# Optimization experiments

Hardware: AMD Instinct MI355X
Metric: run time of the kernel (lower is better)

Reference implementation:

```python
import jax, jax.numpy as jnp
import numpy as np

N, E = 50000, 800000
IN, HID, OUT, HEADS = 256, 128, 256, 4
CAT = HEADS * HID  # 512


def _gat(x, ei_src, ei_dst, W, a_src, a_dst, b, heads, out_ch, concat):
    """PyG-style GATConv with self-loops. x:[N,F]; returns [N,heads*out_ch] or [N,out_ch]."""
    n = x.shape[0]
    loop = jnp.arange(n, dtype=ei_src.dtype)
    src = jnp.concatenate([ei_src, loop])
    dst = jnp.concatenate([ei_dst, loop])
    h = (x @ W).reshape(n, heads, out_ch)              # [N,H,C]
    al_s = jnp.einsum('nhc,hc->nh', h, a_src)          # [N,H]
    al_d = jnp.einsum('nhc,hc->nh', h, a_dst)
    e = jax.nn.leaky_relu(al_s[src] + al_d[dst], 0.2)  # [E',H]
    emax = jax.ops.segment_max(e, dst, num_segments=n)
    ee = jnp.exp(e - emax[dst])
    denom = jax.ops.segment_sum(ee, dst, num_segments=n)
    alpha = ee / (denom[dst] + 1e-16)                  # segment softmax over incoming edges
    out = jax.ops.segment_sum(h[src] * alpha[:, :, None], dst, num_segments=n)  # [N,H,C]
    out = out.reshape(n, heads * out_ch) if concat else out.mean(axis=1)
    return out + b


def setup_inputs() -> dict:
    key = jax.random.key(0)
    ks = jax.random.split(key, 20)
    g = lambda k, shape, fan: (jax.random.normal(k, shape, jnp.float32) / np.sqrt(fan)).astype(jnp.float32)
    return {
        'x': jax.random.normal(ks[0], (N, IN), jnp.float32),
        'edge_index': jax.random.randint(ks[1], (2, E), 0, N, dtype=jnp.int32),
        # GAT layer 1: IN -> HID x 4 heads, concat
        'W1': g(ks[2], (IN, CAT), IN), 'a_src1': g(ks[3], (HEADS, HID), HID),
        'a_dst1': g(ks[4], (HEADS, HID), HID), 'b1': jnp.zeros((CAT,), jnp.float32),
        # GAT layer 2: CAT -> HID x 4 heads, concat
        'W2': g(ks[5], (CAT, CAT), CAT), 'a_src2': g(ks[6], (HEADS, HID), HID),
        'a_dst2': g(ks[7], (HEADS, HID), HID), 'b2': jnp.zeros((CAT,), jnp.float32),
        # GAT layer 3: CAT -> OUT, 1 head, no concat
        'W3': g(ks[8], (CAT, OUT), CAT), 'a_src3': g(ks[9], (1, OUT), OUT),
        'a_dst3': g(ks[10], (1, OUT), OUT), 'b3': jnp.zeros((OUT,), jnp.float32),
        # response_generator MLP: OUT -> 2*HID -> HID -> OUT
        'M1': g(ks[11], (OUT, 2 * HID), OUT), 'mb1': jnp.zeros((2 * HID,), jnp.float32),
        'M2': g(ks[12], (2 * HID, HID), 2 * HID), 'mb2': jnp.zeros((HID,), jnp.float32),
        'M3': g(ks[13], (HID, OUT), HID), 'mb3': jnp.zeros((OUT,), jnp.float32),
    }


def reference(x, edge_index, W1, a_src1, a_dst1, b1, W2, a_src2, a_dst2, b2,
              W3, a_src3, a_dst3, b3, M1, mb1, M2, mb2, M3, mb3):
    src, dst = edge_index[0], edge_index[1]
    h = _gat(x, src, dst, W1, a_src1, a_dst1, b1, HEADS, HID, True)
    h = jax.nn.elu(h)  # dropout is identity in eval mode
    h = _gat(h, src, dst, W2, a_src2, a_dst2, b2, HEADS, HID, True)
    h = jax.nn.elu(h)
    h = _gat(h, src, dst, W3, a_src3, a_dst3, b3, 1, OUT, False)
    # response generator MLP (dropout identity in eval)
    r = jax.nn.relu(h @ M1 + mb1)
    r = jax.nn.relu(r @ M2 + mb2)
    return r @ M3 + mb3
```

## Files before the change

kernel.cpp:

```cpp
#include <hip/hip_runtime.h>
#include <cstdint>
#include <cstddef>

#define HEADS  4
#define HIDC   128
#define CATF   512
#define IN_F   256
#define OUT_F  256

typedef _Float16 f16x8 __attribute__((ext_vector_type(8)));
typedef _Float16 f16x4 __attribute__((ext_vector_type(4)));
typedef float f32x4  __attribute__((ext_vector_type(4)));

__device__ __forceinline__ void async16(const void* g, void* l) {
    __builtin_amdgcn_global_load_lds((const __attribute__((address_space(1))) void*)g,
                                     (__attribute__((address_space(3))) void*)l, 16, 0, 0);
}

__global__ void init_counts(int* cnt, int N) {
    int i = blockIdx.x * blockDim.x + threadIdx.x;
    if (i < N) cnt[i] = 1;
}

__global__ void count_dst(const int* __restrict__ dst, int E, int* cnt) {
    int i = blockIdx.x * blockDim.x + threadIdx.x;
    if (i < E) atomicAdd(&cnt[dst[i]], 1);
}

__global__ void scan_partial(const int* __restrict__ cnt, int* excl, int* bsum, int N) {
    __shared__ int tmp[256];
    int i = blockIdx.x * 256 + threadIdx.x;
    int v = (i < N) ? cnt[i] : 0;
    tmp[threadIdx.x] = v;
    __syncthreads();
    for (int off = 1; off < 256; off <<= 1) {
        int t = ((int)threadIdx.x >= off) ? tmp[threadIdx.x - off] : 0;
        __syncthreads();
        tmp[threadIdx.x] += t;
        __syncthreads();
    }
    if (i < N) excl[i] = tmp[threadIdx.x] - v;
    if (threadIdx.x == 255) bsum[blockIdx.x] = tmp[255];
}

__global__ void scan_bsums(int* bsum, int nb) {
    __shared__ int tmp[256];
    int v = ((int)threadIdx.x < nb) ? bsum[threadIdx.x] : 0;
    tmp[threadIdx.x] = v;
    __syncthreads();
    for (int off = 1; off < 256; off <<= 1) {
        int t = ((int)threadIdx.x >= off) ? tmp[threadIdx.x - off] : 0;
        __syncthreads();
        tmp[threadIdx.x] += t;
        __syncthreads();
    }
    if ((int)threadIdx.x < nb) bsum[threadIdx.x] = tmp[threadIdx.x] - v;
}

__global__ void add_carry(int* indptr, int* pos, const int* __restrict__ bsum, int N, int total) {
    int i = blockIdx.x * blockDim.x + threadIdx.x;
    if (i < N) {
        int v = indptr[i] + bsum[i >> 8];
        indptr[i] = v;
        pos[i] = v;
    }
    if (i == 0) indptr[N] = total;
}

__global__ void scatter_edges(const int* __restrict__ src, const int* __restrict__ dst,
                              int E, int N, int* pos, int* esrc) {
    int i = blockIdx.x * blockDim.x + threadIdx.x;
    int total = E + N;
    if (i >= total) return;
    int s, d;
    if (i < E) { s = src[i]; d = dst[i]; }
    else       { s = i - E;  d = s; }
    int p = atomicAdd(&pos[d], 1);
    esrc[p] = s;
}

__global__ void conv_h16(const float* __restrict__ in, _Float16* __restrict__ out, long n4) {
    long i = (long)blockIdx.x * blockDim.x + threadIdx.x;
    if (i >= n4) return;
    float4 v = ((const float4*)in)[i];
    f16x4 o = { (_Float16)v.x, (_Float16)v.y, (_Float16)v.z, (_Float16)v.w };
    ((f16x4*)out)[i] = o;
}

struct WDesc { const float* W; _Float16* hi; _Float16* lo; int K; int N; int off; };
struct WPack { WDesc d[6]; int total; };
__global__ void conv_w_all(WPack p) {
    int idx = blockIdx.x * blockDim.x + threadIdx.x;
    if (idx >= p.total) return;
    int wi = 0;
    while (wi < 5 && idx >= p.d[wi + 1].off) wi++;
    const WDesc& w = p.d[wi];
    int li = idx - w.off;
    int n = li / w.K, k = li - n * w.K;
    float v = w.W[(size_t)k * w.N + n];
    _Float16 h = (_Float16)v;
    w.hi[(size_t)n * w.K + k] = h;
    if (w.lo) w.lo[(size_t)n * w.K + k] = (_Float16)(v - (float)h);
}

__global__ void zero2(float* a, float* b, int n) {
    int i = blockIdx.x * blockDim.x + threadIdx.x;
    if (i < n) { a[i] = 0.f; b[i] = 0.f; }
}

#define TM 128
#define TN 128
#define TK 32
template <int MODE, int NMF, int ATTN>
__global__ __launch_bounds__(256) void gemm_bt(
        const _Float16* __restrict__ A,
        const _Float16* __restrict__ Bh, const _Float16* __restrict__ Bl,
        const float* __restrict__ bias,
        float* __restrict__ out_f, _Float16* __restrict__ out_h16,
        const float* __restrict__ asrc, const float* __restrict__ adst,
        float* __restrict__ al_s, float* __restrict__ al_d,
        int M, int N, int K, int act) {
    __shared__ __align__(16) _Float16 sA[2][TM * TK], sBh[2][TN * TK];
    __shared__ __align__(16) _Float16 sBl[NMF == 2 ? 2 * TN * TK : 16];
    __shared__ float sred[ATTN ? TM * 4 : 4];
    int tid = threadIdx.x;
    int wave = tid >> 6, lane = tid & 63;
    int m0 = blockIdx.y * TM, n0 = blockIdx.x * TN;
    int wm = wave >> 1, wn = wave & 1;
    int srow = lane >> 2;
    int skel = (lane & 3) * 8;
    int fr = lane & 15, quad = lane >> 4;

    f32x4 acc[4][4];
#pragma unroll
    for (int i = 0; i < 4; i++)
#pragma unroll
        for (int j = 0; j < 4; j++) acc[i][j] = (f32x4){0.f, 0.f, 0.f, 0.f};

    auto stage = [&](int buf, int k0) {
#pragma unroll
        for (int c = 0; c < 2; c++) {
            int chunk = wave * 2 + c;
            int r = chunk * 16 + srow;
            int gmA = m0 + r; if (gmA >= M) gmA = M - 1;
            int gnB = n0 + r;
            size_t aoff = (size_t)gmA * K + k0 + skel;
            size_t boff = (size_t)gnB * K + k0 + skel;
            int ldso = chunk * 512;
            async16(A + aoff, &sA[buf][ldso]);
            async16(Bh + boff, &sBh[buf][ldso]);
            if (NMF == 2) async16(Bl + boff, &sBl[buf * (TN * TK) + ldso]);
        }
    };

    const int nsteps = K / TK;
    stage(0, 0);
    int cur = 0;
    for (int s = 0; s < nsteps; ++s, cur ^= 1) {
        if (s + 1 < nsteps) {
            stage(cur ^ 1, (s + 1) * TK);
            if (NMF == 2) asm volatile("s_waitcnt vmcnt(6)" ::: "memory");
            else          asm volatile("s_waitcnt vmcnt(4)" ::: "memory");
        } else {
            asm volatile("s_waitcnt vmcnt(0)" ::: "memory");
        }
        __builtin_amdgcn_s_barrier();
        __builtin_amdgcn_sched_barrier(0);

        f16x8 fa[4], fbh[4], fbl[4];
#pragma unroll
        for (int i = 0; i < 4; i++) {
            int ra = (wm * 64 + i * 16 + fr) * TK + quad * 8;
            int rb = (wn * 64 + i * 16 + fr) * TK + quad * 8;
            fa[i]  = *(const f16x8*)&sA[cur][ra];
            fbh[i] = *(const f16x8*)&sBh[cur][rb];
            if (NMF == 2) fbl[i] = *(const f16x8*)&sBl[cur * (TN * TK) + rb];
        }
#pragma unroll
        for (int i = 0; i < 4; i++)
#pragma unroll
            for (int j = 0; j < 4; j++) {
                if (NMF == 2)
                    acc[i][j] = __builtin_amdgcn_mfma_f32_16x16x32_f16(fa[i], fbl[j], acc[i][j], 0, 0, 0);
                acc[i][j] = __builtin_amdgcn_mfma_f32_16x16x32_f16(fa[i], fbh[j], acc[i][j], 0, 0, 0);
            }
        __builtin_amdgcn_sched_barrier(0);
        __builtin_amdgcn_s_barrier();
    }

    float avs[4], avd[4];
    if (ATTN) {
#pragma unroll
        for (int j = 0; j < 4; j++) {
            int gn = n0 + wn * 64 + j * 16 + fr;
            avs[j] = asrc[gn];
            avd[j] = adst[gn];
        }
    }

#pragma unroll
    for (int i = 0; i < 4; i++)
#pragma unroll
        for (int r = 0; r < 4; r++) {
            int gm = m0 + wm * 64 + i * 16 + quad * 4 + r;
            if (gm >= M) continue;
            float ps = 0.f, pd = 0.f;
#pragma unroll
            for (int j = 0; j < 4; j++) {
                int gn = n0 + wn * 64 + j * 16 + fr;
                float v = acc[i][j][r];
                if (bias) v += bias[gn];
                if (act == 1) v = fmaxf(v, 0.f);
                size_t o = (size_t)gm * N + gn;
                if (MODE == 1) out_f[o] = v;
                else           out_h16[o] = (_Float16)v;
                if (ATTN) { ps += v * avs[j]; pd += v * avd[j]; }
            }
            if (ATTN) {
#pragma unroll
                for (int off = 1; off < 16; off <<= 1) {
                    ps += __shfl_xor(ps, off);
                    pd += __shfl_xor(pd, off);
                }
                if (fr == 0) {
                    int lrow = wm * 64 + i * 16 + quad * 4 + r;
                    sred[lrow * 4 + 0 * 2 + wn] = ps;
                    sred[lrow * 4 + 1 * 2 + wn] = pd;
                }
            }
        }

    if (ATTN) {
        __syncthreads();
        if (tid < TM) {
            int gm = m0 + tid;
            if (gm < M) {
                float s = sred[tid * 4 + 0] + sred[tid * 4 + 1];
                float d = sred[tid * 4 + 2] + sred[tid * 4 + 3];
                if (ATTN == 1) {
                    int head = n0 >> 7;
                    al_s[gm * HEADS + head] = s;
                    al_d[gm * HEADS + head] = d;
                } else {
                    atomicAdd(&al_s[gm], s);
                    atomicAdd(&al_d[gm], d);
                }
            }
        }
    }
}

template <int CT, int H>
__global__ void gat_aggregate_f(const _Float16* __restrict__ h,
                                const float* __restrict__ al_s, const float* __restrict__ al_d,
                                const int* __restrict__ indptr, const int* __restrict__ esrc,
                                const float* __restrict__ bias,
                                _Float16* __restrict__ oh,
                                int N, int act) {
    typedef _Float16 hvec __attribute__((ext_vector_type(CT)));
    const int C_ALL = CT * 64;
    int n = (blockIdx.x * blockDim.x + threadIdx.x) >> 6;
    int lane = threadIdx.x & 63;
    if (n >= N) return;
    int head = (lane * H) >> 6;
    float ald = al_d[n * H + head];
    float acc[CT];
#pragma unroll
    for (int k = 0; k < CT; k++) acc[k] = 0.f;
    float dsum = 0.f;

    int beg = indptr[n], end = indptr[n + 1];
    int idx = beg;
    for (; idx + 8 <= end; idx += 8) {
        int s[8]; float av[8]; hvec v[8];
#pragma unroll
        for (int u = 0; u < 8; u++) s[u] = esrc[idx + u];
#pragma unroll
        for (int u = 0; u < 8; u++) av[u] = al_s[s[u] * H + head];
#pragma unroll
        for (int u = 0; u < 8; u++) v[u] = *(const hvec*)(h + (size_t)s[u] * C_ALL + lane * CT);
#pragma unroll
        for (int u = 0; u < 8; u++) {
            float e = av[u] + ald;
            e = e > 0.f ? e : 0.2f * e;
            e = fminf(e, 60.f);
            float w = __expf(e);
            dsum += w;
#pragma unroll
            for (int k = 0; k < CT; k++) acc[k] += w * (float)v[u][k];
        }
    }
    if (idx + 4 <= end) {
        int s[4]; float av[4]; hvec v[4];
#pragma unroll
        for (int u = 0; u < 4; u++) s[u] = esrc[idx + u];
#pragma unroll
        for (int u = 0; u < 4; u++) av[u] = al_s[s[u] * H + head];
#pragma unroll
        for (int u = 0; u < 4; u++) v[u] = *(const hvec*)(h + (size_t)s[u] * C_ALL + lane * CT);
#pragma unroll
        for (int u = 0; u < 4; u++) {
            float e = av[u] + ald;
            e = e > 0.f ? e : 0.2f * e;
            e = fminf(e, 60.f);
            float w = __expf(e);
            dsum += w;
#pragma unroll
            for (int k = 0; k < CT; k++) acc[k] += w * (float)v[u][k];
        }
        idx += 4;
    }
    for (; idx < end; idx++) {
        int s0 = esrc[idx];
        float e = al_s[s0 * H + head] + ald;
        e = e > 0.f ? e : 0.2f * e;
        e = fminf(e, 60.f);
        float w = __expf(e);
        dsum += w;
        hvec v0 = *(const hvec*)(h + (size_t)s0 * C_ALL + lane * CT);
#pragma unroll
        for (int k = 0; k < CT; k++) acc[k] += w * (float)v0[k];
    }

    float inv = 1.f / (dsum + 1e-16f);
    size_t ob = (size_t)n * C_ALL + lane * CT;
    const float* bp = bias + lane * CT;
    hvec o;
#pragma unroll
    for (int k = 0; k < CT; k++) {
        float v = acc[k] * inv + bp[k];
        if (act == 1) v = v > 0.f ? v : (__expf(v) - 1.f);
        o[k] = (_Float16)v;
    }
    __builtin_nontemporal_store(o, (hvec*)(oh + ob));
}

extern "C" void kernel_launch(void* const* d_in, const int* in_sizes, int n_in,
                              void* d_out, int out_size, void* d_ws, size_t ws_size,
                              hipStream_t stream) {
    const float* x   = (const float*)d_in[0];
    const int*   ei  = (const int*)d_in[1];
    const float* W1  = (const float*)d_in[2];
    const float* as1 = (const float*)d_in[3];
    const float* ad1 = (const float*)d_in[4];
    const float* b1  = (const float*)d_in[5];
    const float* W2  = (const float*)d_in[6];
    const float* as2 = (const float*)d_in[7];
    const float* ad2 = (const float*)d_in[8];
    const float* b2  = (const float*)d_in[9];
    const float* W3  = (const float*)d_in[10];
    const float* as3 = (const float*)d_in[11];
    const float* ad3 = (const float*)d_in[12];
    const float* b3  = (const float*)d_in[13];
    const float* M1  = (const float*)d_in[14];
    const float* mb1 = (const float*)d_in[15];
    const float* M2  = (const float*)d_in[16];
    const float* mb2 = (const float*)d_in[17];
    const float* M3  = (const float*)d_in[18];
    const float* mb3 = (const float*)d_in[19];
    float* out = (float*)d_out;

    const int N = in_sizes[0] / IN_F;
    const int E = in_sizes[1] / 2;
    const int* src = ei;
    const int* dst = ei + E;

    char* ws = (char*)d_ws;
    auto alloc = [&](size_t bytes) { char* p = ws; ws += (bytes + 255) & ~(size_t)255; return p; };
    _Float16* H16 = (_Float16*)alloc((size_t)N * CATF * 2);
    _Float16* P16 = (_Float16*)alloc((size_t)N * CATF * 2);
    float* al_s = (float*)alloc((size_t)N * HEADS * 4);
    float* al_d = (float*)alloc((size_t)N * HEADS * 4);
    int* cnt    = (int*)alloc((size_t)N * 4);
    int* pos    = (int*)alloc((size_t)N * 4);
    int* indptr = (int*)alloc((size_t)(N + 1) * 4);
    int* esrc   = (int*)alloc((size_t)(E + N) * 4);
    int* bsum   = (int*)alloc(256 * 4);
    auto walloc = [&](int k, int n, _Float16*& h, _Float16*& l, bool need_lo) {
        h = (_Float16*)alloc((size_t)k * n * 2);
        l = need_lo ? (_Float16*)alloc((size_t)k * n * 2) : nullptr;
    };
    _Float16 *W1h, *W1l, *W2h, *W2l, *W3h, *W3l, *M1h, *M1l, *M2h, *M2l, *M3h, *M3l;
    walloc(IN_F, CATF, W1h, W1l, false);
    walloc(CATF, CATF, W2h, W2l, false);
    walloc(CATF, OUT_F, W3h, W3l, false);
    walloc(OUT_F, 2 * HIDC, M1h, M1l, true);
    walloc(2 * HIDC, HIDC, M2h, M2l, true);
    walloc(HIDC, OUT_F, M3h, M3l, true);

    const int nb = (N + 255) / 256;
    init_counts<<<(N + 255) / 256, 256, 0, stream>>>(cnt, N);
    count_dst<<<(E + 255) / 256, 256, 0, stream>>>(dst, E, cnt);
    scan_partial<<<nb, 256, 0, stream>>>(cnt, indptr, bsum, N);
    scan_bsums<<<1, 256, 0, stream>>>(bsum, nb);
    add_carry<<<nb, 256, 0, stream>>>(indptr, pos, bsum, N, E + N);
    scatter_edges<<<(E + N + 255) / 256, 256, 0, stream>>>(src, dst, E, N, pos, esrc);

    {
        WPack p;
        int off = 0;
        auto setd = [&](int i, const float* W, _Float16* h, _Float16* l, int K, int Nc) {
            p.d[i] = WDesc{W, h, l, K, Nc, off};
            off += K * Nc;
        };
        setd(0, W1, W1h, W1l, IN_F, CATF);
        setd(1, W2, W2h, W2l, CATF, CATF);
        setd(2, W3, W3h, W3l, CATF, OUT_F);
        setd(3, M1, M1h, M1l, OUT_F, 2 * HIDC);
        setd(4, M2, M2h, M2l, 2 * HIDC, HIDC);
        setd(5, M3, M3h, M3l, HIDC, OUT_F);
        p.total = off;
        conv_w_all<<<(off + 255) / 256, 256, 0, stream>>>(p);
    }

    auto gemm_gat = [&](const _Float16* Ap, const _Float16* Bhp, _Float16* oh,
                        const float* asrc, const float* adst, int M_, int Nc, int K, int attn_mode) {
        dim3 grid(Nc / TN, (M_ + TM - 1) / TM);
        if (attn_mode == 1)
            gemm_bt<2, 1, 1><<<grid, 256, 0, stream>>>(Ap, Bhp, nullptr, nullptr, nullptr, oh,
                                                       asrc, adst, al_s, al_d, M_, Nc, K, 0);
        else
            gemm_bt<2, 1, 2><<<grid, 256, 0, stream>>>(Ap, Bhp, nullptr, nullptr, nullptr, oh,
                                                       asrc, adst, al_s, al_d, M_, Nc, K, 0);
    };
    auto gemm_mlp16 = [&](const _Float16* Ap, const _Float16* Bhp, const _Float16* Blp,
                          const float* bias, _Float16* oh, int M_, int Nc, int K, int act) {
        dim3 grid(Nc / TN, (M_ + TM - 1) / TM);
        gemm_bt<2, 2, 0><<<grid, 256, 0, stream>>>(Ap, Bhp, Blp, bias, nullptr, oh,
                                                   nullptr, nullptr, nullptr, nullptr, M_, Nc, K, act);
    };

    const int gwav = (N + 3) / 4;

    conv_h16<<<((long)N * IN_F / 4 + 255) / 256, 256, 0, stream>>>(x, P16, (long)N * IN_F / 4);

    gemm_gat(P16, W1h, H16, as1, ad1, N, CATF, IN_F, 1);
    gat_aggregate_f<8, HEADS><<<gwav, 256, 0, stream>>>(H16, al_s, al_d, indptr, esrc,
                                                        b1, P16, N, 1);
    gemm_gat(P16, W2h, H16, as2, ad2, N, CATF, CATF, 1);
    gat_aggregate_f<8, HEADS><<<gwav, 256, 0, stream>>>(H16, al_s, al_d, indptr, esrc,
                                                        b2, P16, N, 1);
    zero2<<<(N + 255) / 256, 256, 0, stream>>>(al_s, al_d, N);
    gemm_gat(P16, W3h, H16, as3, ad3, N, OUT_F, CATF, 2);
    gat_aggregate_f<4, 1><<<gwav, 256, 0, stream>>>(H16, al_s, al_d, indptr, esrc,
                                                    b3, P16, N, 0);
    _Float16* Q16 = H16;
    _Float16* R16 = P16 + (size_t)N * OUT_F;
    gemm_mlp16(P16, M1h, M1l, mb1, Q16, N, 2 * HIDC, OUT_F, 1);
    gemm_mlp16(Q16, M2h, M2l, mb2, R16, N, HIDC, 2 * HIDC, 1);
    {
        dim3 grid(OUT_F / TN, (N + TM - 1) / TM);
        gemm_bt<1, 2, 0><<<grid, 256, 0, stream>>>(R16, M3h, M3l, mb3, out, nullptr,
                                                   nullptr, nullptr, nullptr, nullptr,
                                                   N, OUT_F, HIDC, 0);
    }
}
```

Baseline: 823.4 us.

## Stage fp16 GEMM epilogue through LDS for vectorized stores, remap blocks per XCD

The fp16-output GEMM epilogue now writes results into an XOR-swizzled shared-memory tile and then stores each row with 16-byte vector writes, replacing scattered 2-byte stores. Shared memory is merged into one raw buffer so the epilogue can reuse the A tile region. Workgroup IDs are remapped so consecutive tiles land on the same XCD, aiming for better L2 reuse. Bias is hoisted into registers, and the attention-logit reduction is split from the store loop. The cost is an extra LDS round-trip and barrier in the epilogue.

Measured after the change: 736.3 us. 1.12x faster.

```diff
diff --git a/kernel.cpp b/kernel.cpp
--- a/kernel.cpp
+++ b/kernel.cpp
@@ -120,12 +120,22 @@
         const float* __restrict__ asrc, const float* __restrict__ adst,
         float* __restrict__ al_s, float* __restrict__ al_d,
         int M, int N, int K, int act) {
-    __shared__ __align__(16) _Float16 sA[2][TM * TK], sBh[2][TN * TK];
-    __shared__ __align__(16) _Float16 sBl[NMF == 2 ? 2 * TN * TK : 16];
-    __shared__ float sred[ATTN ? TM * 4 : 4];
+    __shared__ __align__(16) char smem[(NMF == 2 ? 49152 : 32768) + (ATTN ? 2048 : 16)];
+    _Float16* sA  = (_Float16*)smem;
+    _Float16* sBh = (_Float16*)(smem + 16384);
+    _Float16* sBl = (_Float16*)(smem + 32768);
+    float* sred   = (float*)(smem + (NMF == 2 ? 49152 : 32768));
+
     int tid = threadIdx.x;
     int wave = tid >> 6, lane = tid & 63;
-    int m0 = blockIdx.y * TM, n0 = blockIdx.x * TN;
+    int nwg = gridDim.x * gridDim.y;
+    int id  = blockIdx.y * gridDim.x + blockIdx.x;
+    int qq = nwg >> 3, rr = nwg & 7;
+    int xcd = id & 7, li = id >> 3;
+    int wg = (xcd < rr ? xcd * (qq + 1) : rr * (qq + 1) + (xcd - rr) * qq) + li;
+    int by = wg / (int)gridDim.x;
+    int bx = wg - by * (int)gridDim.x;
+    int m0 = by * TM, n0 = bx * TN;
     int wm = wave >> 1, wn = wave & 1;
     int srow = lane >> 2;
     int skel = (lane & 3) * 8;
@@ -146,10 +156,10 @@
             int gnB = n0 + r;
             size_t aoff = (size_t)gmA * K + k0 + skel;
             size_t boff = (size_t)gnB * K + k0 + skel;
-            int ldso = chunk * 512;
-            async16(A + aoff, &sA[buf][ldso]);
-            async16(Bh + boff, &sBh[buf][ldso]);
-            if (NMF == 2) async16(Bl + boff, &sBl[buf * (TN * TK) + ldso]);
+            int ldso = buf * (TM * TK) + chunk * 512;
+            async16(A + aoff, &sA[ldso]);
+            async16(Bh + boff, &sBh[ldso]);
+            if (NMF == 2) async16(Bl + boff, &sBl[ldso]);
         }
     };
 
@@ -170,11 +180,11 @@
         f16x8 fa[4], fbh[4], fbl[4];
 #pragma unroll
         for (int i = 0; i < 4; i++) {
-            int ra = (wm * 64 + i * 16 + fr) * TK + quad * 8;
-            int rb = (wn * 64 + i * 16 + fr) * TK + quad * 8;
-            fa[i]  = *(const f16x8*)&sA[cur][ra];
-            fbh[i] = *(const f16x8*)&sBh[cur][rb];
-            if (NMF == 2) fbl[i] = *(const f16x8*)&sBl[cur * (TN * TK) + rb];
+            int ra = cur * (TM * TK) + (wm * 64 + i * 16 + fr) * TK + quad * 8;
+            int rb = cur * (TN * TK) + (wn * 64 + i * 16 + fr) * TK + quad * 8;
+            fa[i]  = *(const f16x8*)&sA[ra];
+            fbh[i] = *(const f16x8*)&sBh[rb];
+            if (NMF == 2) fbl[i] = *(const f16x8*)&sBl[rb];
         }
 #pragma unroll
         for (int i = 0; i < 4; i++)
@@ -188,35 +198,25 @@
         __builtin_amdgcn_s_barrier();
     }
 
-    float avs[4], avd[4];
+    float avs[4], avd[4], bv[4];
+#pragma unroll
+    for (int j = 0; j < 4; j++) {
+        int gn = n0 + wn * 64 + j * 16 + fr;
+        if (ATTN) { avs[j] = asrc[gn]; avd[j] = adst[gn]; }
+        bv[j] = bias ? bias[gn] : 0.f;
+    }
+
     if (ATTN) {
 #pragma unroll
-        for (int j = 0; j < 4; j++) {
-            int gn = n0 + wn * 64 + j * 16 + fr;
-            avs[j] = asrc[gn];
-            avd[j] = adst[gn];
-        }
-    }
-
-#pragma unroll
-    for (int i = 0; i < 4; i++)
-#pragma unroll
-        for (int r = 0; r < 4; r++) {
-            int gm = m0 + wm * 64 + i * 16 + quad * 4 + r;
-            if (gm >= M) continue;
-            float ps = 0.f, pd = 0.f;
-#pragma unroll
-            for (int j = 0; j < 4; j++) {
-                int gn = n0 + wn * 64 + j * 16 + fr;
-                float v = acc[i][j][r];
-                if (bias) v += bias[gn];
-                if (act == 1) v = fmaxf(v, 0.f);
-                size_t o = (size_t)gm * N + gn;
-                if (MODE == 1) out_f[o] = v;
-                else           out_h16[o] = (_Float16)v;
-                if (ATTN) { ps += v * avs[j]; pd += v * avd[j]; }
-            }
-            if (ATTN) {
+        for (int i = 0; i < 4; i++)
+#pragma unroll
+            for (int r = 0; r < 4; r++) {
+                float ps = 0.f, pd = 0.f;
+#pragma unroll
+                for (int j = 0; j < 4; j++) {
+                    float v = acc[i][j][r];
+                    ps += v * avs[j]; pd += v * avd[j];
+                }
 #pragma unroll
                 for (int off = 1; off < 16; off <<= 1) {
                     ps += __shfl_xor(ps, off);
@@ -228,10 +228,57 @@
                     sred[lrow * 4 + 1 * 2 + wn] = pd;
                 }
             }
-        }
+    }
+
+    if (MODE == 1) {
+#pragma unroll
+        for (int i = 0; i < 4; i++)
+#pragma unroll
+            for (int r = 0; r < 4; r++) {
+                int gm = m0 + wm * 64 + i * 16 + quad * 4 + r;
+                if (gm >= M) continue;
+#pragma unroll
+                for (int j = 0; j < 4; j++) {
+                    int gn = n0 + wn * 64 + j * 16 + fr;
+                    float v = acc[i][j][r] + bv[j];
+                    if (act == 1) v = fmaxf(v, 0.f);
+                    out_f[(size_t)gm * N + gn] = v;
+                }
+            }
+        __syncthreads();
+    } else {
+        _Float16* cst = (_Float16*)smem;
+#pragma unroll
+        for (int i = 0; i < 4; i++) {
+            int svb = ((wm * 16 + i * 4 + quad) << 1) & 15;
+#pragma unroll
+            for (int j = 0; j < 4; j++) {
+#pragma unroll
+                for (int r = 0; r < 4; r++) {
+                    int row = wm * 64 + i * 16 + quad * 4 + r;
+                    int col = wn * 64 + j * 16 + fr;
+                    float v = acc[i][j][r] + bv[j];
+                    if (act == 1) v = fmaxf(v, 0.f);
+                    int blk = (col >> 3) ^ svb;
+                    cst[row * 128 + (blk << 3) + (col & 7)] = (_Float16)v;
+                }
+            }
+        }
+        __syncthreads();
+#pragma unroll
+        for (int q = 0; q < 8; q++) {
+            int c = tid + 256 * q;
+            int row = c >> 4, b = c & 15;
+            int gm = m0 + row;
+            if (gm < M) {
+                int svb = ((row >> 2) << 1) & 15;
+                f16x8 val = *(const f16x8*)&cst[row * 128 + ((b ^ svb) << 3)];
+                *(f16x8*)&out_h16[(size_t)gm * N + n0 + b * 8] = val;
+            }
+        }
+    }
 
     if (ATTN) {
-        __syncthreads();
         if (tid < TM) {
             int gm = m0 + tid;
             if (gm < M) {
```
